# Kernel optimization log

Hardware: AMD Instinct MI355X
Metric: run time of the kernel (lower is better)

## Reference

```python
import jax, jax.numpy as jnp
import numpy as np

N_NODES = 50000
N_EDGES = 800000
HID = 64
N_LAYERS = 4
POS_DIM = 3
PARAM_SCALE = 0.1
POS_HEAD_SCALE = 0.001  # xavier gain=0.001 on final pos Linear


def setup_inputs() -> dict:
    key = jax.random.key(0)
    ks = jax.random.split(key, 12)
    L, H = N_LAYERS, HID
    s = PARAM_SCALE
    return {
        "x": jax.random.normal(ks[0], (N_NODES, HID), jnp.float32),
        "pos": jax.random.normal(ks[1], (N_NODES, POS_DIM), jnp.float32),
        "edge_index": jax.random.randint(ks[2], (2, N_EDGES), 0, N_NODES, jnp.int32),
        # edge MLP: Linear(2H+1 -> H), SiLU, Linear(H -> H), SiLU
        "We1": jax.random.normal(ks[3], (L, 2 * H + 1, H), jnp.float32) * s,
        "be1": jnp.zeros((L, H), jnp.float32),
        "We2": jax.random.normal(ks[4], (L, H, H), jnp.float32) * s,
        "be2": jnp.zeros((L, H), jnp.float32),
        # node MLP: Linear(2H -> H), SiLU, Linear(H -> H)
        "Wn1": jax.random.normal(ks[5], (L, 2 * H, H), jnp.float32) * s,
        "bn1": jnp.zeros((L, H), jnp.float32),
        "Wn2": jax.random.normal(ks[6], (L, H, H), jnp.float32) * s,
        "bn2": jnp.zeros((L, H), jnp.float32),
        # pos MLP: Linear(H -> H), SiLU, Linear(H -> 1) (tiny init)
        "Wp1": jax.random.normal(ks[7], (L, H, H), jnp.float32) * s,
        "bp1": jnp.zeros((L, H), jnp.float32),
        "Wp2": jax.random.normal(ks[8], (L, H, 1), jnp.float32) * POS_HEAD_SCALE,
        "bp2": jnp.zeros((L, 1), jnp.float32),
        # logit(pos_scale=0.5) == 0
        "pos_scale_logit": jnp.zeros((1,), jnp.float32),
    }


def reference(x, pos, edge_index, We1, be1, We2, be2, Wn1, bn1, Wn2, bn2,
              Wp1, bp1, Wp2, bp2, pos_scale_logit):
    POS_CLAMP = 500.0
    POS_UPDATE_CLAMP = 5.0
    src, dst = edge_index[0], edge_index[1]  # messages flow j=src -> i=dst
    n = x.shape[0]
    L = We1.shape[0]

    # pos is NOT fed back between layers in the torch forward, so edge
    # geometry is constant across layers.
    rel = pos[dst] - pos[src]                     # [E, P]
    d2 = jnp.sum(rel * rel, axis=-1, keepdims=True)  # [E, 1]
    deg = jnp.maximum(
        jax.ops.segment_sum(jnp.ones(src.shape, x.dtype), dst, num_segments=n),
        1.0)[:, None]                             # [N, 1]

    pos_new = pos
    for l in range(L):
        # edge MLP on gathered node pairs
        m = jnp.concatenate([x[dst], x[src], d2], axis=-1)  # [E, 2H+1]
        m = jax.nn.silu(m @ We1[l] + be1[l])
        m = jax.nn.silu(m @ We2[l] + be2[l])                # [E, H]
        # scatter-aggregate messages to target nodes
        agg = jax.ops.segment_sum(m, dst, num_segments=n)   # [N, H]
        # node update MLP
        h = jax.nn.silu(jnp.concatenate([x, agg], axis=-1) @ Wn1[l] + bn1[l])
        x = h @ Wn2[l] + bn2[l]
        # position update: mean over incoming edges of rel * phi_pos(m)
        c = jax.nn.silu(m @ Wp1[l] + bp1[l]) @ Wp2[l] + bp2[l]  # [E, 1]
        pos_new = pos + jax.ops.segment_sum(rel * c, dst, num_segments=n) / deg

    upd = (pos_new - pos) * jax.nn.sigmoid(pos_scale_logit[0])
    upd = jnp.clip(upd, -POS_UPDATE_CLAMP, POS_UPDATE_CLAMP)
    pos_out = jnp.clip(pos + upd, -POS_CLAMP, POS_CLAMP)
    return x, pos_out
```

## Files before the change

kernel.cpp:

```cpp
#include <hip/hip_runtime.h>

#define NN 50000
#define NE 800000
#define NTILES 12500
#define TPB 10

typedef __attribute__((ext_vector_type(8))) short short8;
typedef __attribute__((ext_vector_type(4))) float f32x4;

__device__ __forceinline__ float silu_f(float v) {
    return v / (1.0f + __expf(-v));
}
__device__ __forceinline__ unsigned short f2bf(float f) {
    unsigned u = __float_as_uint(f);
    u += 0x7fffu + ((u >> 16) & 1u);
    return (unsigned short)(u >> 16);
}
__device__ __forceinline__ unsigned pk2(float a, float b) {
    return (unsigned)f2bf(a) | ((unsigned)f2bf(b) << 16);
}
__device__ __forceinline__ float bf2f(unsigned short v) {
    return __uint_as_float((unsigned)v << 16);
}
__device__ __forceinline__ void gload_lds16(const unsigned short* g, unsigned short* l) {
    __builtin_amdgcn_global_load_lds(
        (const __attribute__((address_space(1))) unsigned int*)g,
        (__attribute__((address_space(3))) unsigned int*)l, 16, 0, 0);
}
#define FENCE_BAR() do { \
    asm volatile("s_waitcnt lgkmcnt(0)" ::: "memory"); \
    __builtin_amdgcn_sched_barrier(0); \
    __builtin_amdgcn_s_barrier(); \
    __builtin_amdgcn_sched_barrier(0); \
} while (0)
#define VMDRAIN() do { \
    __builtin_amdgcn_sched_barrier(0); \
    asm volatile("s_waitcnt vmcnt(0)" ::: "memory"); \
    __builtin_amdgcn_sched_barrier(0); \
} while (0)

__global__ __launch_bounds__(256) void egnn_hist(
    const int* __restrict__ dst, int* __restrict__ hc)
{
    int e = blockIdx.x * 256 + threadIdx.x;
    if (e < NE) atomicAdd(&hc[dst[e]], 1);
}

__global__ __launch_bounds__(1024) void egnn_scan(
    int* __restrict__ hc, int* __restrict__ rowptr)
{
    __shared__ int part[1024];
    const int t = threadIdx.x;
    const int C = (NN + 1023) / 1024;
    const int b0 = t * C;
    int s = 0;
    for (int i = 0; i < C; ++i) {
        int idx = b0 + i;
        if (idx < NN) s += hc[idx];
    }
    part[t] = s;
    __syncthreads();
    for (int off = 1; off < 1024; off <<= 1) {
        int v = (t >= off) ? part[t - off] : 0;
        __syncthreads();
        part[t] += v;
        __syncthreads();
    }
    int run = part[t] - s;
    for (int i = 0; i < C; ++i) {
        int idx = b0 + i;
        if (idx < NN) {
            int v = hc[idx];
            rowptr[idx] = run;
            hc[idx] = run;
            run += v;
        }
    }
    if (t == 1023) rowptr[NN] = part[1023];
}

__global__ __launch_bounds__(256) void egnn_scatter(
    const int* __restrict__ src, const int* __restrict__ dst,
    const float* __restrict__ pos, int* __restrict__ cursor,
    int* __restrict__ eSrc, int* __restrict__ eDst, float* __restrict__ eD2)
{
    int e = blockIdx.x * 256 + threadIdx.x;
    if (e >= NE) return;
    int s = src[e], d = dst[e];
    float rx = pos[3*d+0] - pos[3*s+0];
    float ry = pos[3*d+1] - pos[3*s+1];
    float rz = pos[3*d+2] - pos[3*s+2];
    int p = atomicAdd(&cursor[d], 1);
    eSrc[p] = s;
    eDst[p] = d;
    eD2[p]  = rx*rx + ry*ry + rz*rz;
}

__global__ __launch_bounds__(256) void egnn_prep_w(
    const float* __restrict__ We1, const float* __restrict__ We2,
    const float* __restrict__ Wp1,
    unsigned short* __restrict__ Wg1, unsigned short* __restrict__ Wg2,
    unsigned short* __restrict__ Wgp1)
{
    int i = blockIdx.x * 256 + threadIdx.x;
    if (i < 4 * 64 * 128) {
        int k = i & 127, n = (i >> 7) & 63, l = i >> 13;
        Wg1[(size_t)(l * 64 + n) * 136 + k] = f2bf(We1[((size_t)l * 129 + k) * 64 + n]);
    }
    if (i < 4 * 64 * 64) {
        int h = i & 63, n = (i >> 6) & 63, l = i >> 12;
        Wg2[(size_t)(l * 64 + n) * 72 + h]  = f2bf(We2[((size_t)l * 64 + h) * 64 + n]);
        Wgp1[(size_t)(l * 64 + n) * 72 + h] = f2bf(Wp1[((size_t)l * 64 + h) * 64 + n]);
    }
}

__global__ __launch_bounds__(256) void egnn_prep_wn(
    const float* __restrict__ Wn1, const float* __restrict__ Wn2,
    unsigned short* __restrict__ Wgn1, unsigned short* __restrict__ Wgn2)
{
    int i = blockIdx.x * 256 + threadIdx.x;
    if (i < 4 * 64 * 128) {
        int k = i & 127, n = (i >> 7) & 63, l = i >> 13;
        Wgn1[(size_t)(l * 64 + n) * 136 + k] = f2bf(Wn1[((size_t)l * 128 + k) * 64 + n]);
    }
    if (i < 4 * 64 * 64) {
        int h = i & 63, n = (i >> 6) & 63, l = i >> 12;
        Wgn2[(size_t)(l * 64 + n) * 72 + h] = f2bf(Wn2[((size_t)l * 64 + h) * 64 + n]);
    }
}

__global__ __launch_bounds__(256) void egnn_xbf(
    const float* __restrict__ x, unsigned short* __restrict__ xbf)
{
    int i = blockIdx.x * 256 + threadIdx.x;
    if (i >= NN * 16) return;
    float4 v = ((const float4*)x)[i];
    ((uint2*)xbf)[i] = make_uint2(pk2(v.x, v.y), pk2(v.z, v.w));
}

template<bool POS>
__global__ __launch_bounds__(256) void egnn_edge(
    const unsigned short* __restrict__ xbf, const float* __restrict__ eD2,
    const int* __restrict__ eSrc, const int* __restrict__ eDst,
    const float* __restrict__ pos,
    const unsigned short* __restrict__ Wg1, const unsigned short* __restrict__ Wg2,
    const unsigned short* __restrict__ Wgp1,
    const float* __restrict__ We1,
    const float* __restrict__ be1, const float* __restrict__ be2,
    const float* __restrict__ bp1, const float* __restrict__ Wp2,
    const float* __restrict__ bp2,
    float* __restrict__ agg, float* __restrict__ dpos, int layer)
{
    __shared__ __align__(16) unsigned char pool[16384 * 2 + 9216 * 2];
    __shared__ int   sS[2][64];
    __shared__ int   sD[2][64];
    __shared__ float s2[2][64];

    unsigned short* const xls0 = (unsigned short*)pool;
    unsigned short* const xls1 = (unsigned short*)(pool + 16384);
    unsigned short* const m1l  = (unsigned short*)(pool + 32768);
    unsigned short* const m2s  = (unsigned short*)(pool + 41984);

    const int t    = threadIdx.x;
    const int lane = t & 63;
    const int w    = t >> 6;
    const int l15  = lane & 15;
    const int g    = lane >> 4;
    const int g4   = g * 4;
    const int eh   = w >> 1;
    const int ch   = w & 1;
    const int er   = lane >> 4;
    const int half = (lane >> 3) & 1;
    const int c    = lane & 7;
    const int tile0 = blockIdx.x * TPB;

    const unsigned short* W1b = &Wg1[(size_t)(layer * 64) * 136];
    const unsigned short* W2b = &Wg2[(size_t)(layer * 64) * 72];
    short8 w1f0[4], w1f1[4], w2f0[2], w2f1[2];
    #pragma unroll
    for (int ks = 0; ks < 4; ++ks) {
        w1f0[ks] = *(const short8*)&W1b[(ch * 32 +      l15) * 136 + ks * 32 + g * 8];
        w1f1[ks] = *(const short8*)&W1b[(ch * 32 + 16 + l15) * 136 + ks * 32 + g * 8];
    }
    #pragma unroll
    for (int ks = 0; ks < 2; ++ks) {
        w2f0[ks] = *(const short8*)&W2b[(ch * 32 +      l15) * 72 + ks * 32 + g * 8];
        w2f1[ks] = *(const short8*)&W2b[(ch * 32 + 16 + l15) * 72 + ks * 32 + g * 8];
    }
    float4 wrv[2], b1v[2], b2v[2];
    {
        const float* Wr = &We1[((size_t)layer * 129 + 128) * 64];
        const float* B1 = &be1[layer * 64];
        const float* B2 = &be2[layer * 64];
        #pragma unroll
        for (int nt = 0; nt < 2; ++nt) {
            int n0 = ch * 32 + nt * 16 + g * 4;
            wrv[nt] = *(const float4*)&Wr[n0];
            b1v[nt] = *(const float4*)&B1[n0];
            b2v[nt] = *(const float4*)&B2[n0];
        }
    }
    float4 b1p[4], w2p[4];
    float bp2v = 0.f;
    if (POS) {
        #pragma unroll
        for (int m = 0; m < 4; ++m) {
            b1p[m] = *(const float4*)&bp1[(size_t)layer * 64 + m * 16 + g4];
            w2p[m] = *(const float4*)&Wp2[(size_t)layer * 64 + m * 16 + g4];
        }
        bp2v = bp2[layer];
    }

    const int* const ip = half ? eSrc : eDst;
    const int ebase = w * 16 + er;

    int nid[4];
    {
        const int gb0 = tile0 * 64;
        #pragma unroll
        for (int i = 0; i < 4; ++i) nid[i] = ip[gb0 + ebase + i * 4];
        #pragma unroll
        for (int i = 0; i < 4; ++i)
            gload_lds16(&xbf[(size_t)nid[i] * 64 + ((c ^ ((ebase + i * 4) & 7)) << 3)],
                        xls0 + w * 2048 + i * 512);
        __builtin_amdgcn_sched_barrier(0);
        #pragma unroll
        for (int i = 0; i < 4; ++i) nid[i] = ip[gb0 + 64 + ebase + i * 4];
        if (t < 64) { sS[0][t] = eSrc[gb0 + t]; sD[0][t] = eDst[gb0 + t]; s2[0][t] = eD2[gb0 + t]; }
    }
    int stS = 0, stD = 0; float st2 = 0.f;
    if (t < 64) {
        const int gb1 = (tile0 + 1) * 64;
        stS = eSrc[gb1 + t]; stD = eDst[gb1 + t]; st2 = eD2[gb1 + t];
    }
    VMDRAIN();
    FENCE_BAR();

    const f32x4 zero = {0.f, 0.f, 0.f, 0.f};

    for (int tt = 0; tt < TPB; ++tt) {
        const int b = tt & 1;
        unsigned short* const xcur = b ? xls1 : xls0;
        unsigned short* const xnxt = b ? xls0 : xls1;

        if (tt + 1 < TPB) {
            #pragma unroll
            for (int i = 0; i < 4; ++i)
                gload_lds16(&xbf[(size_t)nid[i] * 64 + ((c ^ ((ebase + i * 4) & 7)) << 3)],
                            xnxt + w * 2048 + i * 512);
            __builtin_amdgcn_sched_barrier(0);
            if (tt + 2 < TPB) {
                const int gb2 = (tile0 + tt + 2) * 64;
                #pragma unroll
                for (int i = 0; i < 4; ++i) nid[i] = ip[gb2 + ebase + i * 4];
            }
        }

        f32x4 a00 = zero, a01 = zero, a10 = zero, a11 = zero;
        {
            const int r0 = (eh * 32 + l15) * 128;
            const int r1 = r0 + 16 * 128;
            const int r7 = l15 & 7;
            #pragma unroll
            for (int ks = 0; ks < 4; ++ks) {
                int col = (((ks << 2) + g) ^ r7) << 3;
                short8 fb0 = *(const short8*)&xcur[r0 + col];
                short8 fb1 = *(const short8*)&xcur[r1 + col];
                a00 = __builtin_amdgcn_mfma_f32_16x16x32_bf16(w1f0[ks], fb0, a00, 0, 0, 0);
                a01 = __builtin_amdgcn_mfma_f32_16x16x32_bf16(w1f0[ks], fb1, a01, 0, 0, 0);
                a10 = __builtin_amdgcn_mfma_f32_16x16x32_bf16(w1f1[ks], fb0, a10, 0, 0, 0);
                a11 = __builtin_amdgcn_mfma_f32_16x16x32_bf16(w1f1[ks], fb1, a11, 0, 0, 0);
            }
        }
        {
            float d2e0 = s2[b][eh * 32 + l15];
            float d2e1 = s2[b][eh * 32 + 16 + l15];
            int e0 = eh * 32 + l15;
            int e1 = e0 + 16;
            #pragma unroll
            for (int nt = 0; nt < 2; ++nt) {
                int n0 = ch * 32 + nt * 16 + g * 4;
                float4 wr = wrv[nt], bb = b1v[nt];
                f32x4 acc0 = nt ? a10 : a00;
                f32x4 acc1 = nt ? a11 : a01;
                float r0 = silu_f(acc0.x + d2e0 * wr.x + bb.x);
                float r1 = silu_f(acc0.y + d2e0 * wr.y + bb.y);
                float r2 = silu_f(acc0.z + d2e0 * wr.z + bb.z);
                float r3 = silu_f(acc0.w + d2e0 * wr.w + bb.w);
                *(uint2*)&m1l[e0 * 72 + n0] = make_uint2(pk2(r0, r1), pk2(r2, r3));
                r0 = silu_f(acc1.x + d2e1 * wr.x + bb.x);
                r1 = silu_f(acc1.y + d2e1 * wr.y + bb.y);
                r2 = silu_f(acc1.z + d2e1 * wr.z + bb.z);
                r3 = silu_f(acc1.w + d2e1 * wr.w + bb.w);
                *(uint2*)&m1l[e1 * 72 + n0] = make_uint2(pk2(r0, r1), pk2(r2, r3));
            }
        }
        FENCE_BAR();

        f32x4 c00 = zero, c01 = zero, c10 = zero, c11 = zero;
        #pragma unroll
        for (int ks = 0; ks < 2; ++ks) {
            short8 fb0 = *(const short8*)&m1l[(eh * 32 +      l15) * 72 + ks * 32 + g * 8];
            short8 fb1 = *(const short8*)&m1l[(eh * 32 + 16 + l15) * 72 + ks * 32 + g * 8];
            c00 = __builtin_amdgcn_mfma_f32_16x16x32_bf16(w2f0[ks], fb0, c00, 0, 0, 0);
            c01 = __builtin_amdgcn_mfma_f32_16x16x32_bf16(w2f0[ks], fb1, c01, 0, 0, 0);
            c10 = __builtin_amdgcn_mfma_f32_16x16x32_bf16(w2f1[ks], fb0, c10, 0, 0, 0);
            c11 = __builtin_amdgcn_mfma_f32_16x16x32_bf16(w2f1[ks], fb1, c11, 0, 0, 0);
        }

        {
            int e0 = eh * 32 + l15;
            int e1 = e0 + 16;
            #pragma unroll
            for (int nt = 0; nt < 2; ++nt) {
                int n0 = ch * 32 + nt * 16 + g * 4;
                float4 bb = b2v[nt];
                f32x4 acc0 = nt ? c10 : c00;
                f32x4 acc1 = nt ? c11 : c01;
                float r0 = silu_f(acc0.x + bb.x);
                float r1 = silu_f(acc0.y + bb.y);
                float r2 = silu_f(acc0.z + bb.z);
                float r3 = silu_f(acc0.w + bb.w);
                *(uint2*)&m2s[e0 * 72 + n0] = make_uint2(pk2(r0, r1), pk2(r2, r3));
                r0 = silu_f(acc1.x + bb.x);
                r1 = silu_f(acc1.y + bb.y);
                r2 = silu_f(acc1.z + bb.z);
                r3 = silu_f(acc1.w + bb.w);
                *(uint2*)&m2s[e1 * 72 + n0] = make_uint2(pk2(r0, r1), pk2(r2, r3));
            }
        }
        if (tt + 1 < TPB && t < 64) {
            sS[1 - b][t] = stS; sD[1 - b][t] = stD; s2[1 - b][t] = st2;
            if (tt + 2 < TPB) {
                const int gb2 = (tile0 + tt + 2) * 64;
                stS = eSrc[gb2 + t]; stD = eDst[gb2 + t]; st2 = eD2[gb2 + t];
            }
        }
        FENCE_BAR();

        if (POS) {
            f32x4 pa[4] = {zero, zero, zero, zero};
            const unsigned short* WPb = &Wgp1[(size_t)(layer * 64) * 72];
            #pragma unroll
            for (int ks = 0; ks < 2; ++ks) {
                short8 fb = *(const short8*)&m2s[(w * 16 + l15) * 72 + ks * 32 + g * 8];
                #pragma unroll
                for (int m = 0; m < 4; ++m) {
                    short8 wf = *(const short8*)&WPb[(size_t)(m * 16 + l15) * 72 + ks * 32 + g * 8];
                    pa[m] = __builtin_amdgcn_mfma_f32_16x16x32_bf16(wf, fb, pa[m], 0, 0, 0);
                }
            }
            float part = 0.0f;
            #pragma unroll
            for (int m = 0; m < 4; ++m) {
                part += silu_f(pa[m].x + b1p[m].x) * w2p[m].x;
                part += silu_f(pa[m].y + b1p[m].y) * w2p[m].y;
                part += silu_f(pa[m].z + b1p[m].z) * w2p[m].z;
                part += silu_f(pa[m].w + b1p[m].w) * w2p[m].w;
            }
            part += __shfl_xor(part, 16);
            part += __shfl_xor(part, 32);
            if (lane < 16) {
                float cv = part + bp2v;
                int idx16 = w * 16 + lane;
                int d = sD[b][idx16], s = sS[b][idx16];
                float rx = pos[3*d+0] - pos[3*s+0];
                float ry = pos[3*d+1] - pos[3*s+1];
                float rz = pos[3*d+2] - pos[3*s+2];
                atomicAdd(&dpos[3*(size_t)d+0], rx * cv);
                atomicAdd(&dpos[3*(size_t)d+1], ry * cv);
                atomicAdd(&dpos[3*(size_t)d+2], rz * cv);
            }
        }

        VMDRAIN();

        {
            const int e0 = w * 16;
            float v[16];
            #pragma unroll
            for (int i = 0; i < 16; ++i) v[i] = bf2f(m2s[(e0 + i) * 72 + lane]);
            int dd[16];
            #pragma unroll
            for (int i = 0; i < 16; ++i) dd[i] = sD[b][e0 + i];
            float run = v[0];
            int cur = dd[0];
            #pragma unroll
            for (int i = 1; i < 16; ++i) {
                if (dd[i] != cur) {
                    atomicAdd(&agg[(size_t)cur * 64 + lane], run);
                    run = 0.0f;
                    cur = dd[i];
                }
                run += v[i];
            }
            atomicAdd(&agg[(size_t)cur * 64 + lane], run);
        }
        FENCE_BAR();
    }
}

template<bool WRITE_F32>
__global__ __launch_bounds__(256) void egnn_node_mfma(
    const unsigned short* __restrict__ xbf, const float* __restrict__ agg,
    const unsigned short* __restrict__ Wgn1, const unsigned short* __restrict__ Wgn2,
    const float* __restrict__ bn1, const float* __restrict__ bn2,
    float* __restrict__ xout, unsigned short* __restrict__ xbf_out, int layer)
{
    __shared__ __align__(16) unsigned char pool[16384 + 9216];
    unsigned short* const xpl = (unsigned short*)pool;
    unsigned short* const m1l = (unsigned short*)(pool + 16384);
    float* const          sXf = (float*)pool;

    const int t    = threadIdx.x;
    const int lane = t & 63;
    const int w    = t >> 6;
    const int l15  = lane & 15;
    const int g    = lane >> 4;
    const int eh   = w >> 1;
    const int ch   = w & 1;
    const int base = blockIdx.x * 64;
    const int nval = (NN - base < 64) ? (NN - base) : 64;

    #pragma unroll
    for (int i = 0; i < 2; ++i) {
        int e = w * 16 + i * 8 + (lane >> 3);
        int node = base + ((e < nval) ? e : 0);
        gload_lds16(&xbf[(size_t)node * 64 + (((lane & 7) ^ (e & 7)) << 3)],
                    xpl + w * 1024 + i * 512);
    }
    __builtin_amdgcn_sched_barrier(0);

    const unsigned short* W1b = &Wgn1[(size_t)(layer * 64) * 136];
    const unsigned short* W2b = &Wgn2[(size_t)(layer * 64) * 72];
    short8 w1f0[4], w1f1[4], w2f0[2], w2f1[2];
    #pragma unroll
    for (int ks = 0; ks < 4; ++ks) {
        w1f0[ks] = *(const short8*)&W1b[(ch * 32 +      l15) * 136 + ks * 32 + g * 8];
        w1f1[ks] = *(const short8*)&W1b[(ch * 32 + 16 + l15) * 136 + ks * 32 + g * 8];
    }
    #pragma unroll
    for (int ks = 0; ks < 2; ++ks) {
        w2f0[ks] = *(const short8*)&W2b[(ch * 32 +      l15) * 72 + ks * 32 + g * 8];
        w2f1[ks] = *(const short8*)&W2b[(ch * 32 + 16 + l15) * 72 + ks * 32 + g * 8];
    }
    float4 b1v[2], b2v[2];
    {
        const float* B1 = &bn1[layer * 64];
        const float* B2 = &bn2[layer * 64];
        #pragma unroll
        for (int nt = 0; nt < 2; ++nt) {
            int n0 = ch * 32 + nt * 16 + g * 4;
            b1v[nt] = *(const float4*)&B1[n0];
            b2v[nt] = *(const float4*)&B2[n0];
        }
    }

    {
        int e = t >> 2, q = t & 3;
        int node = base + ((e < nval) ? e : 0);
        const float4* ap = (const float4*)&agg[(size_t)node * 64 + q * 16];
        float4 v0 = ap[0], v1 = ap[1], v2 = ap[2], v3 = ap[3];
        uint4 u0, u1;
        u0.x = pk2(v0.x, v0.y); u0.y = pk2(v0.z, v0.w);
        u0.z = pk2(v1.x, v1.y); u0.w = pk2(v1.z, v1.w);
        u1.x = pk2(v2.x, v2.y); u1.y = pk2(v2.z, v2.w);
        u1.z = pk2(v3.x, v3.y); u1.w = pk2(v3.z, v3.w);
        *(uint4*)&xpl[4096 + e * 64 + (((2 * q)     ^ (e & 7)) << 3)] = u0;
        *(uint4*)&xpl[4096 + e * 64 + (((2 * q + 1) ^ (e & 7)) << 3)] = u1;
    }
    __syncthreads();

    const f32x4 zero = {0.f, 0.f, 0.f, 0.f};
    f32x4 a00 = zero, a01 = zero, a10 = zero, a11 = zero;
    {
        const int e0 = eh * 32 + l15;
        const int e1 = e0 + 16;
        const int r7 = e0 & 7;
        #pragma unroll
        for (int ks = 0; ks < 4; ++ks) {
            int kc = (ks << 2) + g;
            int off0 = (kc >> 3) * 4096 + e0 * 64 + (((kc & 7) ^ r7) << 3);
            int off1 = (kc >> 3) * 4096 + e1 * 64 + (((kc & 7) ^ r7) << 3);
            short8 fb0 = *(const short8*)&xpl[off0];
            short8 fb1 = *(const short8*)&xpl[off1];
            a00 = __builtin_amdgcn_mfma_f32_16x16x32_bf16(w1f0[ks], fb0, a00, 0, 0, 0);
            a01 = __builtin_amdgcn_mfma_f32_16x16x32_bf16(w1f0[ks], fb1, a01, 0, 0, 0);
            a10 = __builtin_amdgcn_mfma_f32_16x16x32_bf16(w1f1[ks], fb0, a10, 0, 0, 0);
            a11 = __builtin_amdgcn_mfma_f32_16x16x32_bf16(w1f1[ks], fb1, a11, 0, 0, 0);
        }
    }
    {
        int e0 = eh * 32 + l15;
        int e1 = e0 + 16;
        #pragma unroll
        for (int nt = 0; nt < 2; ++nt) {
            int n0 = ch * 32 + nt * 16 + g * 4;
            float4 bb = b1v[nt];
            f32x4 acc0 = nt ? a10 : a00;
            f32x4 acc1 = nt ? a11 : a01;
            float r0 = silu_f(acc0.x + bb.x);
            float r1 = silu_f(acc0.y + bb.y);
            float r2 = silu_f(acc0.z + bb.z);
            float r3 = silu_f(acc0.w + bb.w);
            *(uint2*)&m1l[e0 * 72 + n0] = make_uint2(pk2(r0, r1), pk2(r2, r3));
            r0 = silu_f(acc1.x + bb.x);
            r1 = silu_f(acc1.y + bb.y);
            r2 = silu_f(acc1.z + bb.z);
            r3 = silu_f(acc1.w + bb.w);
            *(uint2*)&m1l[e1 * 72 + n0] = make_uint2(pk2(r0, r1), pk2(r2, r3));
        }
    }
    __syncthreads();

    f32x4 c00 = zero, c01 = zero, c10 = zero, c11 = zero;
    #pragma unroll
    for (int ks = 0; ks < 2; ++ks) {
        short8 fb0 = *(const short8*)&m1l[(eh * 32 +      l15) * 72 + ks * 32 + g * 8];
        short8 fb1 = *(const short8*)&m1l[(eh * 32 + 16 + l15) * 72 + ks * 32 + g * 8];
        c00 = __builtin_amdgcn_mfma_f32_16x16x32_bf16(w2f0[ks], fb0, c00, 0, 0, 0);
        c01 = __builtin_amdgcn_mfma_f32_16x16x32_bf16(w2f0[ks], fb1, c01, 0, 0, 0);
        c10 = __builtin_amdgcn_mfma_f32_16x16x32_bf16(w2f1[ks], fb0, c10, 0, 0, 0);
        c11 = __builtin_amdgcn_mfma_f32_16x16x32_bf16(w2f1[ks], fb1, c11, 0, 0, 0);
    }
    __syncthreads();

    {
        int e0 = eh * 32 + l15;
        int e1 = e0 + 16;
        #pragma unroll
        for (int nt = 0; nt < 2; ++nt) {
            int n0 = ch * 32 + nt * 16 + g * 4;
            float4 bb = b2v[nt];
            f32x4 acc0 = nt ? c10 : c00;
            f32x4 acc1 = nt ? c11 : c01;
            sXf[e0 * 65 + n0 + 0] = acc0.x + bb.x;
            sXf[e0 * 65 + n0 + 1] = acc0.y + bb.y;
            sXf[e0 * 65 + n0 + 2] = acc0.z + bb.z;
            sXf[e0 * 65 + n0 + 3] = acc0.w + bb.w;
            sXf[e1 * 65 + n0 + 0] = acc1.x + bb.x;
            sXf[e1 * 65 + n0 + 1] = acc1.y + bb.y;
            sXf[e1 * 65 + n0 + 2] = acc1.z + bb.z;
            sXf[e1 * 65 + n0 + 3] = acc1.w + bb.w;
        }
    }
    __syncthreads();

    if (WRITE_F32) {
        #pragma unroll
        for (int i = 0; i < 4; ++i) {
            int idx = i * 256 + t;
            int e = idx >> 4, c = idx & 15;
            if (e < nval) {
                float4 v;
                const float* p = &sXf[e * 65 + c * 4];
                v.x = p[0]; v.y = p[1]; v.z = p[2]; v.w = p[3];
                *reinterpret_cast<float4*>(&xout[(size_t)(base + e) * 64 + c * 4]) = v;
            }
        }
    }
    {
        int e = t >> 2, q = t & 3;
        if (e < nval) {
            const float* p = &sXf[e * 65 + q * 16];
            uint4 u0, u1;
            u0.x = pk2(p[0],  p[1]);  u0.y = pk2(p[2],  p[3]);
            u0.z = pk2(p[4],  p[5]);  u0.w = pk2(p[6],  p[7]);
            u1.x = pk2(p[8],  p[9]);  u1.y = pk2(p[10], p[11]);
            u1.z = pk2(p[12], p[13]); u1.w = pk2(p[14], p[15]);
            *(uint4*)&xbf_out[(size_t)(base + e) * 64 + q * 16 + 0] = u0;
            *(uint4*)&xbf_out[(size_t)(base + e) * 64 + q * 16 + 8] = u1;
        }
    }
}

__global__ __launch_bounds__(256) void egnn_final(
    const float* __restrict__ pos, const float* __restrict__ dpos,
    const int* __restrict__ rowptr, const float* __restrict__ logit,
    float* __restrict__ pos_out)
{
    int i = blockIdx.x * 256 + threadIdx.x;
    if (i >= NN * 3) return;
    int node = i / 3;
    float dg = fmaxf((float)(rowptr[node + 1] - rowptr[node]), 1.0f);
    float sig = 1.0f / (1.0f + __expf(-logit[0]));
    float upd = (dpos[i] / dg) * sig;
    upd = fminf(fmaxf(upd, -5.0f), 5.0f);
    float p = pos[i] + upd;
    pos_out[i] = fminf(fmaxf(p, -500.0f), 500.0f);
}

extern "C" void kernel_launch(void* const* d_in, const int* in_sizes, int n_in,
                              void* d_out, int out_size, void* d_ws, size_t ws_size,
                              hipStream_t stream)
{
    const float* x0    = (const float*)d_in[0];
    const float* pos   = (const float*)d_in[1];
    const int*   src   = (const int*)d_in[2];
    const int*   dst   = src + NE;
    const float* We1   = (const float*)d_in[3];
    const float* be1   = (const float*)d_in[4];
    const float* We2   = (const float*)d_in[5];
    const float* be2   = (const float*)d_in[6];
    const float* Wn1   = (const float*)d_in[7];
    const float* bn1   = (const float*)d_in[8];
    const float* Wn2   = (const float*)d_in[9];
    const float* bn2   = (const float*)d_in[10];
    const float* Wp1   = (const float*)d_in[11];
    const float* bp1   = (const float*)d_in[12];
    const float* Wp2   = (const float*)d_in[13];
    const float* bp2   = (const float*)d_in[14];
    const float* logit = (const float*)d_in[15];

    float* xout    = (float*)d_out;
    float* pos_out = xout + (size_t)NN * 64;

    float* ws  = (float*)d_ws;
    float* agg  = ws;  ws += (size_t)NN * 64;
    float* dpos = ws;  ws += (size_t)NN * 3;
    float* eD2  = ws;  ws += NE;
    int* rowptr = (int*)ws;  ws += NN + 1;
    int* hc     = (int*)ws;  ws += NN;
    int* eSrc   = (int*)ws;  ws += NE;
    int* eDst   = (int*)ws;  ws += NE;
    unsigned short* xbf = (unsigned short*)ws;
    ws += (size_t)NN * 32;
    unsigned short* Wg1  = (unsigned short*)ws;
    unsigned short* Wg2  = Wg1 + 4 * 64 * 136;
    unsigned short* Wgn1 = Wg2 + 4 * 64 * 72;
    unsigned short* Wgn2 = Wgn1 + 4 * 64 * 136;
    unsigned short* Wgp1 = Wgn2 + 4 * 64 * 72;

    hipMemsetAsync(hc, 0, NN * sizeof(int), stream);
    hipMemsetAsync(dpos, 0, (size_t)NN * 3 * sizeof(float), stream);
    egnn_hist<<<NE / 256, 256, 0, stream>>>(dst, hc);
    egnn_scan<<<1, 1024, 0, stream>>>(hc, rowptr);
    egnn_scatter<<<NE / 256, 256, 0, stream>>>(src, dst, pos, hc, eSrc, eDst, eD2);
    egnn_prep_w<<<128, 256, 0, stream>>>(We1, We2, Wp1, Wg1, Wg2, Wgp1);
    egnn_prep_wn<<<128, 256, 0, stream>>>(Wn1, Wn2, Wgn1, Wgn2);
    egnn_xbf<<<(NN * 16 + 255) / 256, 256, 0, stream>>>(x0, xbf);

    const int nblk = NTILES / TPB;
    const int nodeblk = (NN + 63) / 64;
    for (int l = 0; l < 4; ++l) {
        hipMemsetAsync(agg, 0, (size_t)NN * 64 * sizeof(float), stream);
        if (l == 3) {
            egnn_edge<true><<<nblk, 256, 0, stream>>>(
                xbf, eD2, eSrc, eDst, pos, Wg1, Wg2, Wgp1, We1, be1, be2,
                bp1, Wp2, bp2, agg, dpos, l);
            egnn_node_mfma<true><<<nodeblk, 256, 0, stream>>>(
                xbf, agg, Wgn1, Wgn2, bn1, bn2, xout, xbf, l);
        } else {
            egnn_edge<false><<<nblk, 256, 0, stream>>>(
                xbf, eD2, eSrc, eDst, pos, Wg1, Wg2, Wgp1, We1, be1, be2,
                bp1, Wp2, bp2, agg, dpos, l);
            egnn_node_mfma<false><<<nodeblk, 256, 0, stream>>>(
                xbf, agg, Wgn1, Wgn2, bn1, bn2, xout, xbf, l);
        }
    }
    egnn_final<<<(NN * 3 + 255) / 256, 256, 0, stream>>>(pos, dpos, rowptr, logit, pos_out);
}
```

Before: 853.9 us.

## Replace LDS-staged edge metadata with register prefetch and partial vmcnt waits

Per-tile src/dst/d2 metadata now goes straight from global memory into per-lane registers, one tile ahead, instead of being staged through double-buffered LDS arrays. The full vmcnt(0) drains are replaced by hand-counted partial vmcnt waits, so the global-to-LDS gathers and the fire-and-forget atomics can stay in flight across tile boundaries. The segmented scatter reduction becomes branchless, issuing one atomic per edge with a zero when the run continues. In exchange it issues more atomic traffic, reloads 16 dst indices per lane per tile, and relies on fragile hardcoded vmcnt counts that must match the exact instruction schedule.

```diff
diff --git a/kernel.cpp b/kernel.cpp
--- a/kernel.cpp
+++ b/kernel.cpp
@@ -31,11 +31,6 @@
     asm volatile("s_waitcnt lgkmcnt(0)" ::: "memory"); \
     __builtin_amdgcn_sched_barrier(0); \
     __builtin_amdgcn_s_barrier(); \
-    __builtin_amdgcn_sched_barrier(0); \
-} while (0)
-#define VMDRAIN() do { \
-    __builtin_amdgcn_sched_barrier(0); \
-    asm volatile("s_waitcnt vmcnt(0)" ::: "memory"); \
     __builtin_amdgcn_sched_barrier(0); \
 } while (0)
 
@@ -152,10 +147,6 @@
     float* __restrict__ agg, float* __restrict__ dpos, int layer)
 {
     __shared__ __align__(16) unsigned char pool[16384 * 2 + 9216 * 2];
-    __shared__ int   sS[2][64];
-    __shared__ int   sD[2][64];
-    __shared__ float s2[2][64];
-
     unsigned short* const xls0 = (unsigned short*)pool;
     unsigned short* const xls1 = (unsigned short*)(pool + 16384);
     unsigned short* const m1l  = (unsigned short*)(pool + 32768);
@@ -173,6 +164,7 @@
     const int half = (lane >> 3) & 1;
     const int c    = lane & 7;
     const int tile0 = blockIdx.x * TPB;
+    const int wofs16 = __builtin_amdgcn_readfirstlane(w * 16);
 
     const unsigned short* W1b = &Wg1[(size_t)(layer * 64) * 136];
     const unsigned short* W2b = &Wg2[(size_t)(layer * 64) * 72];
@@ -226,15 +218,20 @@
         __builtin_amdgcn_sched_barrier(0);
         #pragma unroll
         for (int i = 0; i < 4; ++i) nid[i] = ip[gb0 + 64 + ebase + i * 4];
-        if (t < 64) { sS[0][t] = eSrc[gb0 + t]; sD[0][t] = eDst[gb0 + t]; s2[0][t] = eD2[gb0 + t]; }
-    }
-    int stS = 0, stD = 0; float st2 = 0.f;
-    if (t < 64) {
-        const int gb1 = (tile0 + 1) * 64;
-        stS = eSrc[gb1 + t]; stD = eDst[gb1 + t]; st2 = eD2[gb1 + t];
-    }
-    VMDRAIN();
-    FENCE_BAR();
+    }
+    float d2c0 = eD2[tile0 * 64 + eh * 32 + l15];
+    float d2c1 = eD2[tile0 * 64 + eh * 32 + 16 + l15];
+    int pD = 0, pS = 0;
+    if (POS) {
+        pD = eDst[tile0 * 64 + wofs16 + l15];
+        pS = eSrc[tile0 * 64 + wofs16 + l15];
+    }
+    __builtin_amdgcn_sched_barrier(0);
+    if (POS) asm volatile("s_waitcnt vmcnt(8)" ::: "memory");
+    else     asm volatile("s_waitcnt vmcnt(6)" ::: "memory");
+    __builtin_amdgcn_sched_barrier(0);
+    __builtin_amdgcn_s_barrier();
+    __builtin_amdgcn_sched_barrier(0);
 
     const f32x4 zero = {0.f, 0.f, 0.f, 0.f};
 
@@ -242,18 +239,26 @@
         const int b = tt & 1;
         unsigned short* const xcur = b ? xls1 : xls0;
         unsigned short* const xnxt = b ? xls0 : xls1;
-
+        const int gb = (tile0 + tt) * 64;
+
+        float d2n0 = 0.f, d2n1 = 0.f;
+        int pDn = 0, pSn = 0;
         if (tt + 1 < TPB) {
+            const int gb1 = gb + 64;
             #pragma unroll
             for (int i = 0; i < 4; ++i)
                 gload_lds16(&xbf[(size_t)nid[i] * 64 + ((c ^ ((ebase + i * 4) & 7)) << 3)],
                             xnxt + w * 2048 + i * 512);
             __builtin_amdgcn_sched_barrier(0);
-            if (tt + 2 < TPB) {
-                const int gb2 = (tile0 + tt + 2) * 64;
-                #pragma unroll
-                for (int i = 0; i < 4; ++i) nid[i] = ip[gb2 + ebase + i * 4];
-            }
+            d2n0 = eD2[gb1 + eh * 32 + l15];
+            d2n1 = eD2[gb1 + eh * 32 + 16 + l15];
+            if (POS) {
+                pDn = eDst[gb1 + wofs16 + l15];
+                pSn = eSrc[gb1 + wofs16 + l15];
+            }
+            const int gb2 = gb + 128;
+            #pragma unroll
+            for (int i = 0; i < 4; ++i) nid[i] = ip[gb2 + ebase + i * 4];
         }
 
         f32x4 a00 = zero, a01 = zero, a10 = zero, a11 = zero;
@@ -273,8 +278,6 @@
             }
         }
         {
-            float d2e0 = s2[b][eh * 32 + l15];
-            float d2e1 = s2[b][eh * 32 + 16 + l15];
             int e0 = eh * 32 + l15;
             int e1 = e0 + 16;
             #pragma unroll
@@ -283,15 +286,15 @@
                 float4 wr = wrv[nt], bb = b1v[nt];
                 f32x4 acc0 = nt ? a10 : a00;
                 f32x4 acc1 = nt ? a11 : a01;
-                float r0 = silu_f(acc0.x + d2e0 * wr.x + bb.x);
-                float r1 = silu_f(acc0.y + d2e0 * wr.y + bb.y);
-                float r2 = silu_f(acc0.z + d2e0 * wr.z + bb.z);
-                float r3 = silu_f(acc0.w + d2e0 * wr.w + bb.w);
+                float r0 = silu_f(acc0.x + d2c0 * wr.x + bb.x);
+                float r1 = silu_f(acc0.y + d2c0 * wr.y + bb.y);
+                float r2 = silu_f(acc0.z + d2c0 * wr.z + bb.z);
+                float r3 = silu_f(acc0.w + d2c0 * wr.w + bb.w);
                 *(uint2*)&m1l[e0 * 72 + n0] = make_uint2(pk2(r0, r1), pk2(r2, r3));
-                r0 = silu_f(acc1.x + d2e1 * wr.x + bb.x);
-                r1 = silu_f(acc1.y + d2e1 * wr.y + bb.y);
-                r2 = silu_f(acc1.z + d2e1 * wr.z + bb.z);
-                r3 = silu_f(acc1.w + d2e1 * wr.w + bb.w);
+                r0 = silu_f(acc1.x + d2c1 * wr.x + bb.x);
+                r1 = silu_f(acc1.y + d2c1 * wr.y + bb.y);
+                r2 = silu_f(acc1.z + d2c1 * wr.z + bb.z);
+                r3 = silu_f(acc1.w + d2c1 * wr.w + bb.w);
                 *(uint2*)&m1l[e1 * 72 + n0] = make_uint2(pk2(r0, r1), pk2(r2, r3));
             }
         }
@@ -329,13 +332,6 @@
                 *(uint2*)&m2s[e1 * 72 + n0] = make_uint2(pk2(r0, r1), pk2(r2, r3));
             }
         }
-        if (tt + 1 < TPB && t < 64) {
-            sS[1 - b][t] = stS; sD[1 - b][t] = stD; s2[1 - b][t] = st2;
-            if (tt + 2 < TPB) {
-                const int gb2 = (tile0 + tt + 2) * 64;
-                stS = eSrc[gb2 + t]; stD = eDst[gb2 + t]; st2 = eD2[gb2 + t];
-            }
-        }
         FENCE_BAR();
 
         if (POS) {
@@ -362,41 +358,46 @@
             part += __shfl_xor(part, 32);
             if (lane < 16) {
                 float cv = part + bp2v;
-                int idx16 = w * 16 + lane;
-                int d = sD[b][idx16], s = sS[b][idx16];
-                float rx = pos[3*d+0] - pos[3*s+0];
-                float ry = pos[3*d+1] - pos[3*s+1];
-                float rz = pos[3*d+2] - pos[3*s+2];
+                int d = pD, s = pS;
+                float rx = pos[3*(size_t)d+0] - pos[3*(size_t)s+0];
+                float ry = pos[3*(size_t)d+1] - pos[3*(size_t)s+1];
+                float rz = pos[3*(size_t)d+2] - pos[3*(size_t)s+2];
                 atomicAdd(&dpos[3*(size_t)d+0], rx * cv);
                 atomicAdd(&dpos[3*(size_t)d+1], ry * cv);
                 atomicAdd(&dpos[3*(size_t)d+2], rz * cv);
             }
         }
 
-        VMDRAIN();
-
         {
-            const int e0 = w * 16;
+            int dd[16];
+            #pragma unroll
+            for (int i = 0; i < 16; ++i) dd[i] = eDst[gb + wofs16 + i];
             float v[16];
             #pragma unroll
-            for (int i = 0; i < 16; ++i) v[i] = bf2f(m2s[(e0 + i) * 72 + lane]);
-            int dd[16];
-            #pragma unroll
-            for (int i = 0; i < 16; ++i) dd[i] = sD[b][e0 + i];
-            float run = v[0];
-            int cur = dd[0];
-            #pragma unroll
-            for (int i = 1; i < 16; ++i) {
-                if (dd[i] != cur) {
-                    atomicAdd(&agg[(size_t)cur * 64 + lane], run);
-                    run = 0.0f;
-                    cur = dd[i];
-                }
+            for (int i = 0; i < 16; ++i) v[i] = bf2f(m2s[(w * 16 + i) * 72 + lane]);
+            float run = 0.0f;
+            #pragma unroll
+            for (int i = 0; i < 16; ++i) {
                 run += v[i];
-            }
-            atomicAdd(&agg[(size_t)cur * 64 + lane], run);
-        }
-        FENCE_BAR();
+                bool bi = (i == 15) || (dd[i + 1] != dd[i]);
+                float ai = bi ? run : 0.0f;
+                atomicAdd(&agg[(size_t)dd[i] * 64 + lane], ai);
+                run = bi ? 0.0f : run;
+            }
+        }
+
+        if (tt + 1 < TPB) {
+            d2c0 = d2n0; d2c1 = d2n1;
+            if (POS) { pD = pDn; pS = pSn; }
+            __builtin_amdgcn_sched_barrier(0);
+            if (POS) asm volatile("s_waitcnt vmcnt(27)" ::: "memory");
+            else     asm volatile("s_waitcnt vmcnt(22)" ::: "memory");
+            __builtin_amdgcn_sched_barrier(0);
+            asm volatile("s_waitcnt lgkmcnt(0)" ::: "memory");
+            __builtin_amdgcn_sched_barrier(0);
+            __builtin_amdgcn_s_barrier();
+            __builtin_amdgcn_sched_barrier(0);
+        }
     }
 }
 
```

Result: slower. 1.387 ms (+62.5%).
